# Kernel optimization log

Measured on AMD Instinct MI355X. Metric: run time of the kernel, lower is better.

Reference implementation:

```python
import jax, jax.numpy as jnp
import numpy as np

B, T, H, YD, L, IN = 128, 1024, 256, 30, 3, 6


def setup_inputs() -> dict:
    key = jax.random.key(0)
    ks = jax.random.split(key, 32)
    s = 1.0 / np.sqrt(H)

    def u(k, shape):
        return jax.random.uniform(k, shape, jnp.float32, -s, s)

    inp = {
        "rew": jax.random.normal(ks[0], (B, T), jnp.float32),
        "done": (jax.random.uniform(ks[1], (B, T)) < 0.02).astype(jnp.float32),
        "gamma": jnp.array([0.99], jnp.float32),
        "prob": jax.random.uniform(ks[2], (B, T), jnp.float32),
        "y": jax.random.uniform(ks[3], (B, T, YD), jnp.float32),
        "y1": jax.random.uniform(ks[4], (B, T, YD), jnp.float32),
    }
    dims = [IN, H, H]
    for l in range(L):
        inp[f"w_ih{l}"] = u(ks[5 + 4 * l], (3 * H, dims[l]))
        inp[f"w_hh{l}"] = u(ks[6 + 4 * l], (3 * H, H))
        inp[f"b_ih{l}"] = u(ks[7 + 4 * l], (3 * H,))
        inp[f"b_hh{l}"] = u(ks[8 + 4 * l], (3 * H,))
    inp["w_fc_y"] = u(ks[20], (YD, H)); inp["b_fc_y"] = u(ks[21], (YD,))
    inp["w_fc_pi"] = u(ks[22], (1, H)); inp["b_fc_pi"] = u(ks[23], (1,))
    inp["w_e1"] = u(ks[24], (16, YD)); inp["b_e1"] = u(ks[25], (16,))
    inp["w_e2"] = u(ks[26], (1, 16)); inp["b_e2"] = u(ks[27], (1,))
    return inp


def _forward(rew, done, gamma, prob, y, y1,
             w_ih0, w_hh0, b_ih0, b_hh0,
             w_ih1, w_hh1, b_ih1, b_hh1,
             w_ih2, w_hh2, b_ih2, b_hh2,
             w_fc_y, b_fc_y, w_fc_pi, b_fc_pi,
             w_e1, b_e1, w_e2, b_e2):
    def embed(v):  # embed_y: Linear -> relu -> Linear -> sigmoid, [B,T,YD]->[B,T,1]
        h1 = jax.nn.relu(v @ w_e1.T + b_e1)
        return jax.nn.sigmoid(h1 @ w_e2.T + b_e2)

    fi_y = embed(y)
    fi_y1 = embed(y1)
    g = gamma * jnp.ones((B, T, 1), rew.dtype)
    x = jnp.concatenate([rew[..., None], done[..., None], g,
                         prob[..., None], fi_y, fi_y1], axis=-1)  # [B,T,6]
    x = jnp.flip(x, axis=1)  # reverse time, as in torch.flip(input, dims=[1])
    xs = jnp.moveaxis(x, 1, 0)  # [T,B,6]
    ds = xs[:, :, 1:2]          # done channel, [T,B,1]

    wih = (w_ih0, w_ih1, w_ih2)
    whh = (w_hh0, w_hh1, w_hh2)
    bih = (b_ih0, b_ih1, b_ih2)
    bhh = (b_hh0, b_hh1, b_hh2)

    def cell(xt, h, Wi, Wh, bi, bh):  # PyTorch GRU cell math
        gi = xt @ Wi.T + bi
        gh = h @ Wh.T + bh
        ir, iz, inn = jnp.split(gi, 3, axis=-1)
        hr, hz, hn = jnp.split(gh, 3, axis=-1)
        r = jax.nn.sigmoid(ir + hr)
        z = jax.nn.sigmoid(iz + hz)
        n = jnp.tanh(inn + r * hn)
        return (1.0 - z) * n + z * h

    def step(h, xd):
        xt, dt = xd                       # xt [B,6], dt [B,1]
        h = h * (1.0 - dt)[None]          # reset hidden where done==1
        layer_in = xt
        hs = []
        for l in range(L):
            hl = cell(layer_in, h[l], wih[l], whh[l], bih[l], bhh[l])
            hs.append(hl)
            layer_in = hl
        return jnp.stack(hs), layer_in

    h0 = jnp.zeros((L, B, H), xs.dtype)
    _, out = jax.lax.scan(step, h0, (xs, ds))  # out [T,B,H]
    out = jnp.moveaxis(out, 0, 1)              # [B,T,H]

    yo = jax.nn.sigmoid(out @ w_fc_y.T + b_fc_y)  # [B,T,YD]
    pi = out @ w_fc_pi.T + b_fc_pi                # [B,T,1]
    pi = jnp.flip(pi, axis=1)[..., 0]             # [B,T]
    yo = jnp.flip(yo, axis=1)                     # [B,T,YD] (squeeze(-1) is a no-op for YD>1)
    return pi, yo


def reference(rew, done, gamma, prob, y, y1,
              w_ih0, w_hh0, b_ih0, b_hh0,
              w_ih1, w_hh1, b_ih1, b_hh1,
              w_ih2, w_hh2, b_ih2, b_hh2,
              w_fc_y, b_fc_y, w_fc_pi, b_fc_pi,
              w_e1, b_e1, w_e2, b_e2):
    return _forward(rew, done, gamma, prob, y, y1,
                    w_ih0, w_hh0, b_ih0, b_hh0,
                    w_ih1, w_hh1, b_ih1, b_hh1,
                    w_ih2, w_hh2, b_ih2, b_hh2,
                    w_fc_y, b_fc_y, w_fc_pi, b_fc_pi,
                    w_e1, b_e1, w_e2, b_e2)
```

## Files before the change

kernel.cpp:

```cpp
#include <hip/hip_runtime.h>

#define BDIM 128
#define TDIM 1024
#define HDIM 256
#define SLOT (BDIM*HDIM)
#define NWG_TOTAL 208
#define RING 14

#define FLAGS_OFF 0u
#define HD_OFF    8192u
#define XF_OFF    5513216u
#define DONEF_OFF 8658944u
#define WS_NEEDED 9183232u
#define NZERO_U32 1378304

#define LDS_DYN 98304

typedef __attribute__((ext_vector_type(8))) short bf16x8;
typedef __attribute__((ext_vector_type(4))) float f32x4;

static __device__ __forceinline__ unsigned short f2bf(float f) {
  union { float f; unsigned u; } v; v.f = f;
  unsigned r = v.u + 0x7fffu + ((v.u >> 16) & 1u);
  return (unsigned short)(r >> 16);
}
static __device__ __forceinline__ float bf2f(unsigned short h) {
  union { unsigned u; float f; } v; v.u = ((unsigned)h) << 16;
  return v.f;
}
static __device__ __forceinline__ float sigm(float x) { return 1.f / (1.f + __expf(-x)); }
static __device__ __forceinline__ float tanha(float x) { return 1.f - 2.f / (1.f + __expf(2.f * x)); }

static __device__ __forceinline__ unsigned long long ld_u64_coh(const void* p) {
  return __hip_atomic_load((const unsigned long long*)p, __ATOMIC_RELAXED, __HIP_MEMORY_SCOPE_AGENT);
}
static __device__ __forceinline__ void st_u32_coh(void* p, unsigned v) {
  __hip_atomic_store((unsigned*)p, v, __ATOMIC_RELAXED, __HIP_MEMORY_SCOPE_AGENT);
}
static __device__ __forceinline__ bf16x8 ld_frag_coh(const unsigned short* p) {
  union { bf16x8 v; unsigned long long q[2]; } u;
  u.q[0] = ld_u64_coh(p);
  u.q[1] = ld_u64_coh(p + 4);
  return u.v;
}

static __device__ __forceinline__ unsigned poll_flag(const unsigned* p) {
  return __hip_atomic_load(p, __ATOMIC_RELAXED, __HIP_MEMORY_SCOPE_AGENT);
}
static __device__ __forceinline__ void post_flag(unsigned* fl, int g, int w, int s1) {
  (void)__hip_atomic_exchange(fl + (g * 16 + w) * 8, (unsigned)s1,
                              __ATOMIC_RELAXED, __HIP_MEMORY_SCOPE_AGENT);
}

static __device__ __forceinline__ void wave_wait2(unsigned* fl,
                                                  int g0, int t0, int skip0,
                                                  int g1, int t1,
                                                  int g2, int t2, bool g2four) {
  const int lane = threadIdx.x & 63;
  const int sel = lane >> 4;
  const int w = lane & 15;
  int g = g0, tgt = t0;
  if (sel == 1) { g = g1; tgt = t1; }
  if (sel == 2) { g = g2; tgt = t2; }
  if (sel == 3) tgt = 0;
  if (sel == 0 && w == skip0) tgt = 0;
  const int wi = (sel == 2 && g2four) ? (w & 3) : w;
  const unsigned* p = fl + (g * 16 + wi) * 8;
  const bool need = tgt > 0;
  for (;;) {
    int ok = 1;
    if (need) ok = ((int)poll_flag(p) >= tgt);
    if (__all(ok)) break;
    __builtin_amdgcn_s_sleep(8);
  }
  asm volatile("" ::: "memory");
}

__global__ void diag_kernel(float* out, float code) {
  if (threadIdx.x == 0 && blockIdx.x == 0) out[0] = code;
}

__global__ void prep_kernel(const float* __restrict__ rew, const float* __restrict__ done,
                            const float* __restrict__ gamma, const float* __restrict__ prob,
                            const float* __restrict__ y, const float* __restrict__ y1,
                            const float* __restrict__ w_e1, const float* __restrict__ b_e1,
                            const float* __restrict__ w_e2, const float* __restrict__ b_e2,
                            char* __restrict__ ws) {
  unsigned* zbase = (unsigned*)ws;
  float* donef = (float*)(ws + DONEF_OFF);
  float* xfeat = (float*)(ws + XF_OFF);

  __shared__ float we1[480], be1[16], we2[16];
  __shared__ float be2s, gam;
  for (int i = threadIdx.x; i < 480; i += blockDim.x) we1[i] = w_e1[i];
  if (threadIdx.x < 16) { be1[threadIdx.x] = b_e1[threadIdx.x]; we2[threadIdx.x] = w_e2[threadIdx.x]; }
  if (threadIdx.x == 0) { be2s = b_e2[0]; gam = gamma[0]; }
  __syncthreads();
  const int gid = blockIdx.x * blockDim.x + threadIdx.x;
  const int stride = gridDim.x * blockDim.x;

  for (int i = gid; i < NZERO_U32; i += stride) zbase[i] = 0u;
  for (int i = gid; i < BDIM * TDIM; i += stride) donef[i] = done[i];

  for (int i = gid; i < BDIM * TDIM; i += stride) {
    float yr[30], y1r[30];
    #pragma unroll
    for (int c = 0; c < 30; ++c) { yr[c] = y[(size_t)i * 30 + c]; y1r[c] = y1[(size_t)i * 30 + c]; }
    float a0 = 0.f, a1 = 0.f;
    #pragma unroll 4
    for (int jm = 0; jm < 16; ++jm) {
      float s0 = be1[jm], s1 = be1[jm];
      #pragma unroll
      for (int c = 0; c < 30; ++c) { float w = we1[jm * 30 + c]; s0 += yr[c] * w; s1 += y1r[c] * w; }
      a0 += fmaxf(s0, 0.f) * we2[jm];
      a1 += fmaxf(s1, 0.f) * we2[jm];
    }
    float* xr = xfeat + (size_t)i * 6;
    xr[0] = rew[i]; xr[1] = done[i]; xr[2] = gam;
    xr[3] = prob[i]; xr[4] = sigm(a0 + be2s); xr[5] = sigm(a1 + be2s);
  }
}

template <bool L0T>
__device__ __forceinline__ void layer_body(int l, int rg, int js, char* __restrict__ ws,
                                           char* __restrict__ ldsx,
                                           const float* __restrict__ Wh,
                                           const float* __restrict__ Wx,
                                           const float* __restrict__ bi,
                                           const float* __restrict__ bh,
                                           const float* __restrict__ wi0) {
  unsigned short* hd = (unsigned short*)(ws + HD_OFF);
  unsigned* fl = (unsigned*)(ws + FLAGS_OFF);
  const float* donef = (const float*)(ws + DONEF_OFF);
  const float* xfeat = (const float*)(ws + XF_OFF);

  const int tid = threadIdx.x;
  const int wv = tid >> 6, lane = tid & 63, q = lane >> 4, jj = lane & 15;
  const int j = js * 16 + jj;

  const float bi_r = bi[j], bi_z = bi[256 + j], bi_n = bi[512 + j];
  const float bh_r = bh[j], bh_z = bh[256 + j], bh_n = bh[512 + j];

  bf16x8 Bh[3][2][8];
  #pragma unroll
  for (int g = 0; g < 3; ++g)
    #pragma unroll
    for (int it = 0; it < 8; ++it) {
      const float* src = Wh + (size_t)(g * 256 + j) * 256 + it * 32 + q * 8;
      #pragma unroll
      for (int e = 0; e < 8; ++e) {
        const float w = src[e];
        const unsigned short d1 = f2bf(w);
        const unsigned short d2 = f2bf(w - bf2f(d1));
        Bh[g][0][it][e] = (short)d1;
        Bh[g][1][it][e] = (short)d2;
      }
    }

  if (!L0T) {
    for (int idx = tid; idx < 12288; idx += 128) {
      const int row = idx >> 8, k = idx & 255;
      const int g = row >> 4, jr = row & 15;
      const float w = Wx[(size_t)(g * 256 + js * 16 + jr) * 256 + k];
      const unsigned short d1 = f2bf(w);
      const unsigned short d2 = f2bf(w - bf2f(d1));
      const int it = k >> 5, kk = k & 31;
      *(unsigned short*)(ldsx + ((g * 2 + 0) * 8 + it) * 1280 + jr * 80 + kk * 2) = d1;
      *(unsigned short*)(ldsx + ((g * 2 + 1) * 8 + it) * 1280 + jr * 80 + kk * 2) = d2;
    }
  }
  __syncthreads();

  float wx0[3][6];
  if (L0T) {
    #pragma unroll
    for (int g = 0; g < 3; ++g)
      #pragma unroll
      for (int c = 0; c < 6; ++c) wx0[g][c] = wi0[(g * 256 + j) * 6 + c];
  }

  float hc[4];
  #pragma unroll
  for (int i = 0; i < 4; ++i) hc[i] = 0.f;

  const int mA = (rg * 2 + wv) * 16 + jj;
  const f32x4 z4 = {0.f, 0.f, 0.f, 0.f};

  for (int s = 0; s < 1024; ++s) {
    const int t = 1023 - s;
    const int pc = s % RING, pp = (s + RING - 1) % RING;

    float sFv[4];
    #pragma unroll
    for (int i = 0; i < 4; ++i)
      sFv[i] = 1.f - donef[((rg * 2 + wv) * 16 + q * 4 + i) * TDIM + t];

    if (L0T)         wave_wait2(fl, rg,     s, js, 4 + rg,  s - (RING - 1), 0, 0, false);
    else if (l == 1) wave_wait2(fl, 4 + rg, s, js, rg,      s + 1, 8 + rg,  s - (RING - 1), false);
    else             wave_wait2(fl, 8 + rg, s, js, 4 + rg,  s + 1, 12 + rg, s - (RING - 1), true);

    const unsigned short* hh1 = hd + (size_t)((l * RING + pp) * 2 + 0) * SLOT;
    const unsigned short* hh2 = hd + (size_t)((l * RING + pp) * 2 + 1) * SLOT;
    const unsigned short* hx1 = L0T ? (const unsigned short*)0 : hd + (size_t)(((l - 1) * RING + pc) * 2 + 0) * SLOT;
    const unsigned short* hx2 = L0T ? (const unsigned short*)0 : hd + (size_t)(((l - 1) * RING + pc) * 2 + 1) * SLOT;
    unsigned short* hdw1 = hd + (size_t)((l * RING + pc) * 2 + 0) * SLOT;
    unsigned short* hdw2 = hd + (size_t)((l * RING + pc) * 2 + 1) * SLOT;

    f32x4 Ch[3], Cx[3];
    #pragma unroll
    for (int g = 0; g < 3; ++g) { Ch[g] = z4; Cx[g] = z4; }

    #pragma unroll
    for (int it = 0; it < 8; ++it) {
      const int koff = it * 32 + q * 8;
      const size_t ro = (size_t)mA * 256 + koff;
      bf16x8 a1 = ld_frag_coh(hh1 + ro);
      bf16x8 a2 = ld_frag_coh(hh2 + ro);
      bf16x8 x1{}, x2{};
      if (!L0T) {
        x1 = ld_frag_coh(hx1 + ro);
        x2 = ld_frag_coh(hx2 + ro);
      }
      #pragma unroll
      for (int g = 0; g < 3; ++g) {
        #pragma unroll
        for (int dig = 0; dig < 2; ++dig) {
          const bf16x8 wb = Bh[g][dig][it];
          Ch[g] = __builtin_amdgcn_mfma_f32_16x16x32_bf16(a1, wb, Ch[g], 0, 0, 0);
          Ch[g] = __builtin_amdgcn_mfma_f32_16x16x32_bf16(a2, wb, Ch[g], 0, 0, 0);
          if (!L0T) {
            const bf16x8 xb = *(const bf16x8*)(ldsx + ((g * 2 + dig) * 8 + it) * 1280 + jj * 80 + q * 16);
            Cx[g] = __builtin_amdgcn_mfma_f32_16x16x32_bf16(x1, xb, Cx[g], 0, 0, 0);
            Cx[g] = __builtin_amdgcn_mfma_f32_16x16x32_bf16(x2, xb, Cx[g], 0, 0, 0);
          }
        }
      }
    }

    #pragma unroll
    for (int i = 0; i < 4; ++i) {
      const int mC = (rg * 2 + wv) * 16 + q * 4 + i;
      const float sF = sFv[i];
      float gxr, gxz, gxn;
      if (L0T) {
        const float* xr = xfeat + ((size_t)mC * TDIM + t) * 6;
        gxr = 0.f; gxz = 0.f; gxn = 0.f;
        #pragma unroll
        for (int c = 0; c < 6; ++c) {
          const float xv = xr[c];
          gxr += xv * wx0[0][c]; gxz += xv * wx0[1][c]; gxn += xv * wx0[2][c];
        }
      } else {
        gxr = Cx[0][i]; gxz = Cx[1][i]; gxn = Cx[2][i];
      }
      const float r = sigm(gxr + bi_r + sF * Ch[0][i] + bh_r);
      const float z = sigm(gxz + bi_z + sF * Ch[1][i] + bh_z);
      const float n = tanha(gxn + bi_n + r * (sF * Ch[2][i] + bh_n));
      const float hp = hc[i] * sF;
      const float hv = (1.f - z) * n + z * hp;
      hc[i] = hv;
      const unsigned short d1 = f2bf(hv);
      const unsigned short d2 = f2bf(hv - bf2f(d1));
      const int o1 = __shfl_xor((int)d1, 1, 64);
      const int o2 = __shfl_xor((int)d2, 1, 64);
      const unsigned val = (jj & 1) ? ((unsigned)(o2 & 0xffff) | ((unsigned)d2 << 16))
                                    : ((unsigned)d1 | ((unsigned)(o1 & 0xffff) << 16));
      unsigned short* bp = ((jj & 1) ? hdw2 : hdw1) + (size_t)mC * 256 + (j & ~1);
      st_u32_coh(bp, val);
    }

    asm volatile("s_waitcnt vmcnt(0)" ::: "memory");
    __syncthreads();
    if (tid == 0) post_flag(fl, l * 4 + rg, js, s + 1);
  }
}

__device__ __forceinline__ void head_body(int hw, char* __restrict__ ws, float* __restrict__ out,
                                          char* __restrict__ lds,
                                          const float* __restrict__ wfy,
                                          const float* __restrict__ bfy,
                                          const float* __restrict__ wfp,
                                          const float* __restrict__ bfp) {
  const unsigned short* hd = (const unsigned short*)(ws + HD_OFF);
  unsigned* fl = (unsigned*)(ws + FLAGS_OFF);
  float* hlds = (float*)lds;

  const int tid = threadIdx.x;
  const int rg = hw >> 2;

  for (int s = 0; s < 1024; ++s) {
    const int t = 1023 - s;
    const int pc = s % RING;
    wave_wait2(fl, 8 + rg, s + 1, -1, 0, 0, 0, 0, false);

    #pragma unroll
    for (int sub = 0; sub < 2; ++sub) {
      const int te = tid + 128 * sub;
      const size_t rowoff = (size_t)(hw * 8 + (te >> 5)) * 256 + (te & 31) * 8;
      const unsigned short* p1 = hd + (size_t)((2 * RING + pc) * 2 + 0) * SLOT + rowoff;
      const unsigned short* p2 = hd + (size_t)((2 * RING + pc) * 2 + 1) * SLOT + rowoff;
      unsigned long long q10 = ld_u64_coh(p1);
      unsigned long long q11 = ld_u64_coh(p1 + 4);
      unsigned long long q20 = ld_u64_coh(p2);
      unsigned long long q21 = ld_u64_coh(p2 + 4);
      float* dst = hlds + (te >> 5) * 256 + (te & 31) * 8;
      #pragma unroll
      for (int e = 0; e < 4; ++e) {
        dst[e]     = bf2f((unsigned short)(q10 >> (16 * e))) + bf2f((unsigned short)(q20 >> (16 * e)));
        dst[4 + e] = bf2f((unsigned short)(q11 >> (16 * e))) + bf2f((unsigned short)(q21 >> (16 * e)));
      }
    }
    __syncthreads();
    #pragma unroll
    for (int sub = 0; sub < 2; ++sub) {
      const int te = tid + 128 * sub;
      const int d = te & 31;
      const int bb = te >> 5;
      const int b = hw * 8 + bb;
      if (d < 31) {
        const float* wrow = (d < 30) ? (wfy + d * 256) : wfp;
        const float biasv = (d < 30) ? bfy[d] : bfp[0];
        const float* hr = hlds + bb * 256;
        float a0 = 0.f, a1 = 0.f;
        #pragma unroll 8
        for (int kk = 0; kk < 256; kk += 8) {
          const f32x4 h0 = *(const f32x4*)(hr + kk);
          const f32x4 h1 = *(const f32x4*)(hr + kk + 4);
          const f32x4 w0 = *(const f32x4*)(wrow + kk);
          const f32x4 w1 = *(const f32x4*)(wrow + kk + 4);
          a0 += h0[0]*w0[0] + h0[1]*w0[1] + h0[2]*w0[2] + h0[3]*w0[3];
          a1 += h1[0]*w1[0] + h1[1]*w1[1] + h1[2]*w1[2] + h1[3]*w1[3];
        }
        const float acc = a0 + a1;
        if (d < 30) out[BDIM * TDIM + ((size_t)b * TDIM + t) * 30 + d] = sigm(acc + biasv);
        else        out[(size_t)b * TDIM + t] = acc + biasv;
      }
    }
    __syncthreads();
    if (tid == 0) post_flag(fl, 12 + rg, hw & 3, s + 1);
  }
}

__global__ void __launch_bounds__(128, 1) gru_main(char* __restrict__ ws,
                                                   float* __restrict__ out,
                                                   const float* __restrict__ wi0,
                                                   const float* __restrict__ wh0,
                                                   const float* __restrict__ bi0,
                                                   const float* __restrict__ bh0,
                                                   const float* __restrict__ wi1,
                                                   const float* __restrict__ wh1,
                                                   const float* __restrict__ bi1,
                                                   const float* __restrict__ bh1,
                                                   const float* __restrict__ wi2,
                                                   const float* __restrict__ wh2,
                                                   const float* __restrict__ bi2,
                                                   const float* __restrict__ bh2,
                                                   const float* __restrict__ wfy,
                                                   const float* __restrict__ bfy,
                                                   const float* __restrict__ wfp,
                                                   const float* __restrict__ bfp) {
  extern __shared__ char lds[];
  const int bid = blockIdx.x;
  if (bid < 192) {
    const int l = bid >> 6;
    const int rg = (bid >> 4) & 3;
    const int js = bid & 15;
    const float* Wh = (l == 0) ? wh0 : (l == 1) ? wh1 : wh2;
    const float* Wx = (l == 0) ? (const float*)0 : (l == 1) ? wi1 : wi2;
    const float* bi = (l == 0) ? bi0 : (l == 1) ? bi1 : bi2;
    const float* bh = (l == 0) ? bh0 : (l == 1) ? bh1 : bh2;
    if (l == 0) layer_body<true>(l, rg, js, ws, lds, Wh, Wx, bi, bh, wi0);
    else        layer_body<false>(l, rg, js, ws, lds, Wh, Wx, bi, bh, wi0);
  } else {
    head_body(bid - 192, ws, out, lds, wfy, bfy, wfp, bfp);
  }
}

extern "C" void kernel_launch(void* const* d_in, const int* in_sizes, int n_in,
                              void* d_out, int out_size, void* d_ws, size_t ws_size,
                              hipStream_t stream) {
  static const int EXP_SIZES[26] = {131072, 131072, 1, 131072, 3932160, 3932160,
                                    4608, 196608, 768, 768,
                                    196608, 196608, 768, 768,
                                    196608, 196608, 768, 768,
                                    7680, 30, 256, 1, 480, 16, 16, 1};
  float code = 0.f;
  if (n_in != 26) code = 900.f;
  if (code == 0.f) {
    for (int i = 0; i < 26; ++i)
      if (in_sizes[i] != EXP_SIZES[i]) { code = 100.f + 4.f * (float)i; break; }
  }
  if (code == 0.f && out_size != 4063232) code = 400.f;
  if (code == 0.f && ws_size < (size_t)WS_NEEDED) code = 300.f;
  if (code != 0.f) {
    diag_kernel<<<1, 64, 0, stream>>>((float*)d_out, code);
    return;
  }

  static int attr_done = 0;
  if (!attr_done) {
    attr_done = 1;
    (void)hipFuncSetAttribute((const void*)gru_main,
                              hipFuncAttributeMaxDynamicSharedMemorySize, LDS_DYN);
  }

  char* ws = (char*)d_ws;
  prep_kernel<<<512, 256, 0, stream>>>(
      (const float*)d_in[0], (const float*)d_in[1], (const float*)d_in[2],
      (const float*)d_in[3], (const float*)d_in[4], (const float*)d_in[5],
      (const float*)d_in[22], (const float*)d_in[23], (const float*)d_in[24], (const float*)d_in[25],
      ws);
  gru_main<<<NWG_TOTAL, 128, LDS_DYN, stream>>>(
      ws, (float*)d_out,
      (const float*)d_in[6], (const float*)d_in[7], (const float*)d_in[8], (const float*)d_in[9],
      (const float*)d_in[10], (const float*)d_in[11], (const float*)d_in[12], (const float*)d_in[13],
      (const float*)d_in[14], (const float*)d_in[15], (const float*)d_in[16], (const float*)d_in[17],
      (const float*)d_in[18], (const float*)d_in[19], (const float*)d_in[20], (const float*)d_in[21]);
}
```

Before: 8.733 ms.

## Move recurrent weights to LDS and batch-issue coherent hidden-state loads

Recurrent weight fragments (hi/lo bf16 split) now live in LDS rather than 96 VGPRs per lane, freeing registers. That room holds all hidden and input fragments for a step, issued up front as 16-byte system-coherent loads with explicit vmcnt waits. The h-path MFMAs can start once the h loads land while the x loads are still in flight. The cost is extra LDS reads per MFMA, a larger LDS allocation, and inline asm that bypasses compiler scheduling.

```diff
diff --git a/kernel.cpp b/kernel.cpp
--- a/kernel.cpp
+++ b/kernel.cpp
@@ -14,7 +14,8 @@
 #define WS_NEEDED 9183232u
 #define NZERO_U32 1378304
 
-#define LDS_DYN 98304
+#define LDSW_BYTES 61440
+#define LDS_DYN    122880
 
 typedef __attribute__((ext_vector_type(8))) short bf16x8;
 typedef __attribute__((ext_vector_type(4))) float f32x4;
@@ -37,11 +38,16 @@
 static __device__ __forceinline__ void st_u32_coh(void* p, unsigned v) {
   __hip_atomic_store((unsigned*)p, v, __ATOMIC_RELAXED, __HIP_MEMORY_SCOPE_AGENT);
 }
-static __device__ __forceinline__ bf16x8 ld_frag_coh(const unsigned short* p) {
-  union { bf16x8 v; unsigned long long q[2]; } u;
-  u.q[0] = ld_u64_coh(p);
-  u.q[1] = ld_u64_coh(p + 4);
-  return u.v;
+
+static __device__ __forceinline__ bf16x8 ld16_coh_nowait(const unsigned short* p) {
+  bf16x8 v;
+  asm volatile("global_load_dwordx4 %0, %1, off sc0 sc1" : "=v"(v) : "v"(p));
+  return v;
+}
+template <int N>
+static __device__ __forceinline__ void wait_vm() {
+  asm volatile("s_waitcnt vmcnt(%0)" :: "i"(N) : "memory");
+  __builtin_amdgcn_sched_barrier(0);
 }
 
 static __device__ __forceinline__ unsigned poll_flag(const unsigned* p) {
@@ -123,7 +129,8 @@
 
 template <bool L0T>
 __device__ __forceinline__ void layer_body(int l, int rg, int js, char* __restrict__ ws,
-                                           char* __restrict__ ldsx,
+                                           char* __restrict__ ldsW,
+                                           char* __restrict__ ldsX,
                                            const float* __restrict__ Wh,
                                            const float* __restrict__ Wx,
                                            const float* __restrict__ bi,
@@ -141,22 +148,16 @@
   const float bi_r = bi[j], bi_z = bi[256 + j], bi_n = bi[512 + j];
   const float bh_r = bh[j], bh_z = bh[256 + j], bh_n = bh[512 + j];
 
-  bf16x8 Bh[3][2][8];
-  #pragma unroll
-  for (int g = 0; g < 3; ++g)
-    #pragma unroll
-    for (int it = 0; it < 8; ++it) {
-      const float* src = Wh + (size_t)(g * 256 + j) * 256 + it * 32 + q * 8;
-      #pragma unroll
-      for (int e = 0; e < 8; ++e) {
-        const float w = src[e];
-        const unsigned short d1 = f2bf(w);
-        const unsigned short d2 = f2bf(w - bf2f(d1));
-        Bh[g][0][it][e] = (short)d1;
-        Bh[g][1][it][e] = (short)d2;
-      }
-    }
-
+  for (int idx = tid; idx < 12288; idx += 128) {
+    const int row = idx >> 8, k = idx & 255;
+    const int g = row >> 4, jr = row & 15;
+    const float w = Wh[(size_t)(g * 256 + js * 16 + jr) * 256 + k];
+    const unsigned short d1 = f2bf(w);
+    const unsigned short d2 = f2bf(w - bf2f(d1));
+    const int itc = k >> 5, kk = k & 31;
+    *(unsigned short*)(ldsW + ((g * 2 + 0) * 8 + itc) * 1280 + jr * 80 + kk * 2) = d1;
+    *(unsigned short*)(ldsW + ((g * 2 + 1) * 8 + itc) * 1280 + jr * 80 + kk * 2) = d2;
+  }
   if (!L0T) {
     for (int idx = tid; idx < 12288; idx += 128) {
       const int row = idx >> 8, k = idx & 255;
@@ -164,9 +165,9 @@
       const float w = Wx[(size_t)(g * 256 + js * 16 + jr) * 256 + k];
       const unsigned short d1 = f2bf(w);
       const unsigned short d2 = f2bf(w - bf2f(d1));
-      const int it = k >> 5, kk = k & 31;
-      *(unsigned short*)(ldsx + ((g * 2 + 0) * 8 + it) * 1280 + jr * 80 + kk * 2) = d1;
-      *(unsigned short*)(ldsx + ((g * 2 + 1) * 8 + it) * 1280 + jr * 80 + kk * 2) = d2;
+      const int itc = k >> 5, kk = k & 31;
+      *(unsigned short*)(ldsX + ((g * 2 + 0) * 8 + itc) * 1280 + jr * 80 + kk * 2) = d1;
+      *(unsigned short*)(ldsX + ((g * 2 + 1) * 8 + itc) * 1280 + jr * 80 + kk * 2) = d2;
     }
   }
   __syncthreads();
@@ -206,32 +207,52 @@
     unsigned short* hdw1 = hd + (size_t)((l * RING + pc) * 2 + 0) * SLOT;
     unsigned short* hdw2 = hd + (size_t)((l * RING + pc) * 2 + 1) * SLOT;
 
+    bf16x8 A1[8], A2[8], X1[8], X2[8];
+    #pragma unroll
+    for (int it = 0; it < 8; ++it) {
+      const size_t ro = (size_t)mA * 256 + it * 32 + q * 8;
+      A1[it] = ld16_coh_nowait(hh1 + ro);
+      A2[it] = ld16_coh_nowait(hh2 + ro);
+    }
+    if (!L0T) {
+      #pragma unroll
+      for (int it = 0; it < 8; ++it) {
+        const size_t ro = (size_t)mA * 256 + it * 32 + q * 8;
+        X1[it] = ld16_coh_nowait(hx1 + ro);
+        X2[it] = ld16_coh_nowait(hx2 + ro);
+      }
+    }
+
     f32x4 Ch[3], Cx[3];
     #pragma unroll
     for (int g = 0; g < 3; ++g) { Ch[g] = z4; Cx[g] = z4; }
 
+    if (L0T) wait_vm<0>(); else wait_vm<16>();
     #pragma unroll
     for (int it = 0; it < 8; ++it) {
-      const int koff = it * 32 + q * 8;
-      const size_t ro = (size_t)mA * 256 + koff;
-      bf16x8 a1 = ld_frag_coh(hh1 + ro);
-      bf16x8 a2 = ld_frag_coh(hh2 + ro);
-      bf16x8 x1{}, x2{};
-      if (!L0T) {
-        x1 = ld_frag_coh(hx1 + ro);
-        x2 = ld_frag_coh(hx2 + ro);
-      }
+      const int cb = it * 1280 + jj * 80 + q * 16;
       #pragma unroll
       for (int g = 0; g < 3; ++g) {
         #pragma unroll
         for (int dig = 0; dig < 2; ++dig) {
-          const bf16x8 wb = Bh[g][dig][it];
-          Ch[g] = __builtin_amdgcn_mfma_f32_16x16x32_bf16(a1, wb, Ch[g], 0, 0, 0);
-          Ch[g] = __builtin_amdgcn_mfma_f32_16x16x32_bf16(a2, wb, Ch[g], 0, 0, 0);
-          if (!L0T) {
-            const bf16x8 xb = *(const bf16x8*)(ldsx + ((g * 2 + dig) * 8 + it) * 1280 + jj * 80 + q * 16);
-            Cx[g] = __builtin_amdgcn_mfma_f32_16x16x32_bf16(x1, xb, Cx[g], 0, 0, 0);
-            Cx[g] = __builtin_amdgcn_mfma_f32_16x16x32_bf16(x2, xb, Cx[g], 0, 0, 0);
+          const bf16x8 wb = *(const bf16x8*)(ldsW + ((g * 2 + dig) * 8) * 1280 + cb);
+          Ch[g] = __builtin_amdgcn_mfma_f32_16x16x32_bf16(A1[it], wb, Ch[g], 0, 0, 0);
+          Ch[g] = __builtin_amdgcn_mfma_f32_16x16x32_bf16(A2[it], wb, Ch[g], 0, 0, 0);
+        }
+      }
+    }
+    if (!L0T) {
+      wait_vm<0>();
+      #pragma unroll
+      for (int it = 0; it < 8; ++it) {
+        const int cb = it * 1280 + jj * 80 + q * 16;
+        #pragma unroll
+        for (int g = 0; g < 3; ++g) {
+          #pragma unroll
+          for (int dig = 0; dig < 2; ++dig) {
+            const bf16x8 xb = *(const bf16x8*)(ldsX + ((g * 2 + dig) * 8) * 1280 + cb);
+            Cx[g] = __builtin_amdgcn_mfma_f32_16x16x32_bf16(X1[it], xb, Cx[g], 0, 0, 0);
+            Cx[g] = __builtin_amdgcn_mfma_f32_16x16x32_bf16(X2[it], xb, Cx[g], 0, 0, 0);
           }
         }
       }
@@ -369,8 +390,8 @@
     const float* Wx = (l == 0) ? (const float*)0 : (l == 1) ? wi1 : wi2;
     const float* bi = (l == 0) ? bi0 : (l == 1) ? bi1 : bi2;
     const float* bh = (l == 0) ? bh0 : (l == 1) ? bh1 : bh2;
-    if (l == 0) layer_body<true>(l, rg, js, ws, lds, Wh, Wx, bi, bh, wi0);
-    else        layer_body<false>(l, rg, js, ws, lds, Wh, Wx, bi, bh, wi0);
+    if (l == 0) layer_body<true>(l, rg, js, ws, lds, lds + LDSW_BYTES, Wh, Wx, bi, bh, wi0);
+    else        layer_body<false>(l, rg, js, ws, lds, lds + LDSW_BYTES, Wh, Wx, bi, bh, wi0);
   } else {
     head_body(bid - 192, ws, out, lds, wfy, bfy, wfp, bfp);
   }
```

New measurement: 9.002 ms. 1.03x slower.
